# Performance work log

Hardware: AMD Instinct MI355X
Metric: run time of the kernel (lower is better)

## Reference

```python
import jax, jax.numpy as jnp
import numpy as np

B, L, H, TE = 256, 2048, 64, 64  # batch, seq len, hidden_size, num_time_enc_dims


def _lin_init(k, out_d, in_d):
    bound = 1.0 / np.sqrt(in_d)
    kw, kb = jax.random.split(k)
    w = jax.random.uniform(kw, (out_d, in_d), jnp.float32, -bound, bound)
    b = jax.random.uniform(kb, (out_d,), jnp.float32, -bound, bound)
    return w, b


def setup_inputs() -> dict:
    key = jax.random.key(0)
    ks = jax.random.split(key, 16)
    x_xy = jax.random.normal(ks[0], (B, L, 2), jnp.float32)
    mask = jax.random.bernoulli(ks[1], 0.8, (B, L, 1)).astype(jnp.float32)  # 0 => masked position
    x = jnp.concatenate([x_xy, mask], axis=-1)  # (B,L,3)
    t = jax.random.uniform(ks[2], (B, L, 1), jnp.float32)
    te_w1, te_b1 = _lin_init(ks[3], TE, 1)
    te_w2, te_b2 = _lin_init(ks[4], TE, TE)
    fproj_w, fproj_b = _lin_init(ks[5], H, 3 + TE)
    bproj_w, bproj_b = _lin_init(ks[6], H, 3 + TE)
    fwz, fbz = _lin_init(ks[7], H, H)
    fwh, fbh = _lin_init(ks[8], H, H)
    bwz, bbz = _lin_init(ks[9], H, H)
    bwh, bbh = _lin_init(ks[10], H, H)
    head_hidden = max((2 * H + TE) // 2, 128)  # = 128
    gh_w1, gh_b1 = _lin_init(ks[11], head_hidden, 2 * H + TE)
    gh_w2, gh_b2 = _lin_init(ks[12], 1, head_hidden)
    mask_token = jnp.array([0.0, 0.01], jnp.float32) + jnp.array([0.1, 0.001], jnp.float32) * jax.random.normal(ks[13], (2,), jnp.float32)
    return dict(x=x, t=t, mask_token=mask_token,
                te_w1=te_w1, te_b1=te_b1, te_w2=te_w2, te_b2=te_b2,
                fproj_w=fproj_w, fproj_b=fproj_b, bproj_w=bproj_w, bproj_b=bproj_b,
                fwz=fwz, fbz=fbz, fwh=fwh, fbh=fbh,
                bwz=bwz, bbz=bbz, bwh=bwh, bbh=bbh,
                gh_w1=gh_w1, gh_b1=gh_b1, gh_w2=gh_w2, gh_b2=gh_b2)


def _mingru_prestates(inp, wz, bz, wh, bh, reverse):
    # inp: (B,L,H). Returns the hidden state BEFORE each step's update, in
    # time order, matching the torch code which stores h_* before cell.step.
    z = jax.nn.sigmoid(jnp.einsum('blh,oh->blo', inp, wz) + bz)
    h_tilde = jnp.tanh(jnp.einsum('blh,oh->blo', inp, wh) + bh)

    def step(h, zh):
        z_t, ht_t = zh
        return (1.0 - z_t) * h + z_t * ht_t, h  # emit pre-update carry

    h0 = jnp.zeros((inp.shape[0], wz.shape[0]), inp.dtype)
    _, hs = jax.lax.scan(step, h0,
                         (jnp.swapaxes(z, 0, 1), jnp.swapaxes(h_tilde, 0, 1)),
                         reverse=reverse)
    return jnp.swapaxes(hs, 0, 1)  # (B,L,H)


def reference(x, t, mask_token,
              te_w1, te_b1, te_w2, te_b2,
              fproj_w, fproj_b, bproj_w, bproj_b,
              fwz, fbz, fwh, fbh,
              bwz, bbz, bwh, bbh,
              gh_w1, gh_b1, gh_w2, gh_b2):
    mask_chan = x[..., 2:3]                      # (B,L,1)
    masked_pos = mask_chan == 0
    x_first2 = jnp.where(masked_pos, mask_token.reshape(1, 1, 2), x[..., :2])
    x3 = jnp.concatenate([x_first2, mask_chan], axis=-1)  # (B,L,3)

    t_enc = jax.nn.relu(jnp.einsum('blk,ok->blo', t, te_w1) + te_b1)
    t_enc = jnp.einsum('blk,ok->blo', t_enc, te_w2) + te_b2  # (B,L,TE)

    x_cat = jnp.concatenate([x3, t_enc], axis=-1)  # (B,L,3+TE)

    inp_fwd = jnp.einsum('blk,ok->blo', x_cat, fproj_w) + fproj_b
    inp_bwd = jnp.einsum('blk,ok->blo', x_cat, bproj_w) + bproj_b

    h_fwd = _mingru_prestates(inp_fwd, fwz, fbz, fwh, fbh, reverse=False)  # state after steps 0..t-1
    h_bwd = _mingru_prestates(inp_bwd, bwz, bbz, bwh, bbh, reverse=True)   # state after steps L-1..t+1

    h_fwd_final = h_fwd[:, -1:, :]  # state after steps 0..L-2
    h_bwd_final = h_bwd[:, 0:1, :]  # state after steps L-1..1

    unmasked = mask_chan > 0
    h_fwd_apply = jnp.where(unmasked, h_fwd, h_fwd_final)
    h_bwd_apply = jnp.where(unmasked, h_bwd, h_bwd_final)

    h_bi = jnp.concatenate([h_fwd_apply, h_bwd_apply, t_enc], axis=-1)  # (B,L,2H+TE)
    hid = jax.nn.relu(jnp.einsum('blk,ok->blo', h_bi, gh_w1) + gh_b1)
    preds = jnp.einsum('blk,ok->blo', hid, gh_w2) + gh_b2  # (B,L,1)
    return preds
```

## Files before the change

### kernel.cpp

```cpp
#include <hip/hip_runtime.h>
#include <stdint.h>

#define NB 256
#define NL 2048

typedef __attribute__((ext_vector_type(8))) short short8;
typedef __attribute__((ext_vector_type(4))) float f32x4;
#define MFMA16(a,b,c) __builtin_amdgcn_mfma_f32_16x16x32_bf16(a,b,c,0,0,0)

static __device__ __forceinline__ unsigned short f2bf(float f) {
    union { float f; uint32_t u; } v; v.f = f;
    uint32_t u = v.u;
    uint32_t r = u + 0x7fffu + ((u >> 16) & 1u);
    return (unsigned short)(r >> 16);
}
static __device__ __forceinline__ float bflo(uint32_t u) {
    union { uint32_t u; float f; } v; v.u = u << 16; return v.f;
}
static __device__ __forceinline__ float bfhi(uint32_t u) {
    union { uint32_t u; float f; } v; v.u = u & 0xffff0000u; return v.f;
}
#if __has_builtin(__builtin_amdgcn_cvt_pk_bf16_f32)
typedef __attribute__((ext_vector_type(2))) __bf16 bf16x2_t;
static __device__ __forceinline__ uint32_t pk2(float lo, float hi) {
    union { bf16x2_t v; uint32_t u; } c;
    c.v = __builtin_amdgcn_cvt_pk_bf16_f32(lo, hi);
    return c.u;
}
static __device__ __forceinline__ unsigned short bf1(float v) {
    union { bf16x2_t v; uint32_t u; } c;
    c.v = __builtin_amdgcn_cvt_pk_bf16_f32(v, v);
    return (unsigned short)(c.u & 0xffffu);
}
#else
static __device__ __forceinline__ uint32_t pk2(float lo, float hi) {
    return ((uint32_t)f2bf(hi) << 16) | (uint32_t)f2bf(lo);
}
static __device__ __forceinline__ unsigned short bf1(float v) { return f2bf(v); }
#endif
static __device__ __forceinline__ short8 frag8(const float* p) {
    short8 r;
#pragma unroll
    for (int j = 0; j < 8; ++j) r[j] = (short)f2bf(p[j]);
    return r;
}

static __device__ __forceinline__ void barrier_lds() {
    asm volatile("s_waitcnt lgkmcnt(0)" ::: "memory");
    __builtin_amdgcn_s_barrier();
}

__global__ __launch_bounds__(256, 3) void prep_kernel(
    const float* __restrict__ x, const float* __restrict__ t,
    const float* __restrict__ mtok,
    const float* __restrict__ te_w1, const float* __restrict__ te_b1,
    const float* __restrict__ te_w2, const float* __restrict__ te_b2,
    const float* __restrict__ fpw, const float* __restrict__ fpb,
    const float* __restrict__ bpw, const float* __restrict__ bpb,
    int b0,
    unsigned short* __restrict__ inpF,
    unsigned short* __restrict__ inpB)
{
    __shared__ __align__(16) unsigned short s_te1[64*72];
    __shared__ __align__(16) unsigned short s_tenc[64*72];
    __shared__ __align__(16) unsigned short s_xa[64*40];
    __shared__ __align__(16) unsigned short s_inp[2][64*72];

    const int tid = threadIdx.x;
    const int w   = tid >> 6;
    const int l   = tid & 63;
    const int lq  = l >> 4;
    const int ln  = l & 15;

    short8 bte[2];
    {
        const float* row = te_w2 + (w*16 + ln)*64;
#pragma unroll
        for (int ks = 0; ks < 2; ++ks) bte[ks] = frag8(row + lq*8 + ks*32);
    }
    short8 bpj[2][3];
#pragma unroll
    for (int p = 0; p < 2; ++p) {
        const int g = 2*w + p;
        const float* PW = (g < 4) ? fpw : bpw;
        const float* row = PW + ((g & 3)*16 + ln)*67;
#pragma unroll
        for (int ks = 0; ks < 2; ++ks) {
            float tmp[8];
#pragma unroll
            for (int j = 0; j < 8; ++j) tmp[j] = row[3 + lq*8 + ks*32 + j];
            bpj[p][ks] = frag8(tmp);
        }
        {
            float tmp[8];
#pragma unroll
            for (int j = 0; j < 8; ++j) tmp[j] = (lq == 0 && j < 3) ? row[j] : 0.f;
            bpj[p][2] = frag8(tmp);
        }
    }
    const float bias_te = te_b2[w*16 + ln];
    float bias_pj[2];
#pragma unroll
    for (int p = 0; p < 2; ++p) {
        const int g = 2*w + p;
        bias_pj[p] = ((g < 4) ? fpb : bpb)[(g & 3)*16 + ln];
    }
    const float mt0 = mtok[0], mt1 = mtok[1];

    const int baseposl = blockIdx.x * 256;

    auto P0 = [&](int ch) {
        const int gbase = (b0 << 11) + baseposl + ch*64;
        const int pos = tid & 63;
        const float tv = t[gbase + pos];
        const int k0 = (tid >> 6) * 16;
        uint32_t* dst = (uint32_t*)(s_te1 + pos*72 + k0);
#pragma unroll
        for (int kk = 0; kk < 16; kk += 2) {
            float v0 = fmaxf(fmaf(tv, te_w1[k0+kk],   te_b1[k0+kk]),   0.f);
            float v1 = fmaxf(fmaf(tv, te_w1[k0+kk+1], te_b1[k0+kk+1]), 0.f);
            dst[kk >> 1] = pk2(v0, v1);
        }
        if (tid < 64) {
            const float* xp = x + (size_t)(gbase + tid)*3;
            const float mc = xp[2];
            const float x0 = (mc == 0.f) ? mt0 : xp[0];
            const float x1 = (mc == 0.f) ? mt1 : xp[1];
            uint32_t* xr = (uint32_t*)(s_xa + tid*40);
            xr[0] = pk2(x0, x1);
            xr[1] = pk2(mc, 0.f);
        }
    };
    auto G1 = [&]() {
        const int o = w*16 + ln;
#pragma unroll
        for (int mt = 0; mt < 4; ++mt) {
            f32x4 c = {0.f, 0.f, 0.f, 0.f};
#pragma unroll
            for (int ks = 0; ks < 2; ++ks) {
                const short8 a = *(const short8*)(s_te1 + (mt*16+ln)*72 + lq*8 + ks*32);
                c = MFMA16(a, bte[ks], c);
            }
#pragma unroll
            for (int r = 0; r < 4; ++r) {
                const int m = mt*16 + lq*4 + r;
                s_tenc[m*72 + o] = bf1(c[r] + bias_te);
            }
        }
    };
    auto G2 = [&]() {
#pragma unroll
        for (int mt = 0; mt < 4; ++mt) {
            short8 a0 = *(const short8*)(s_tenc + (mt*16+ln)*72 + lq*8);
            short8 a1 = *(const short8*)(s_tenc + (mt*16+ln)*72 + lq*8 + 32);
            short8 a2 = *(const short8*)(s_xa   + (mt*16+ln)*40 + lq*8);
#pragma unroll
            for (int p = 0; p < 2; ++p) {
                const int g = 2*w + p;
                const int dir = g >> 2;
                const int o = (g & 3)*16 + ln;
                f32x4 c = {0.f, 0.f, 0.f, 0.f};
                c = MFMA16(a0, bpj[p][0], c);
                c = MFMA16(a1, bpj[p][1], c);
                c = MFMA16(a2, bpj[p][2], c);
#pragma unroll
                for (int r = 0; r < 4; ++r) {
                    const int m = mt*16 + lq*4 + r;
                    s_inp[dir][m*72 + o] = bf1(c[r] + bias_pj[p]);
                }
            }
        }
    };
    auto S = [&](int ch) {
        const int chbase = baseposl + ch*64;
        const int ll0 = chbase & 2047;
        const int bl  = chbase >> 11;
        uint32_t* dstF = (uint32_t*)inpF + ((size_t)bl*NL + ll0)*32;
        uint32_t* dstB = (uint32_t*)inpB + ((size_t)bl*NL + ll0)*32;
        const uint32_t* srcW = (const uint32_t*)s_inp;
#pragma unroll
        for (int rep = 0; rep < 16; ++rep) {
            const int idx = rep*256 + tid;
            const int d   = idx >> 11;
            const int rem = idx & 2047;
            const int ll  = rem >> 5;
            const int dw  = rem & 31;
            const uint32_t v = srcW[d*2304 + ll*36 + dw];
            (d ? dstB : dstF)[ll*32 + dw] = v;
        }
    };

#pragma unroll
    for (int i = tid; i < 64*20; i += 256) {
        if ((i % 20) >= 2) ((uint32_t*)s_xa)[i] = 0;
    }
    P0(0);
    barrier_lds();
    G1();
    barrier_lds();
    G2();
    barrier_lds();
#pragma unroll 1
    for (int ch = 0; ch < 4; ++ch) {
        S(ch);
        if (ch < 3) P0(ch + 1);
        barrier_lds();
        if (ch < 3) {
            G1();
            barrier_lds();
            G2();
            barrier_lds();
        }
    }
}

#define SSTR 129

__global__ __launch_bounds__(512, 2) void scan3_kernel(
    const unsigned short* __restrict__ inpf, const unsigned short* __restrict__ inpb,
    const float* __restrict__ fwz, const float* __restrict__ fbz,
    const float* __restrict__ fwh, const float* __restrict__ fbh,
    const float* __restrict__ bwz, const float* __restrict__ bbz,
    const float* __restrict__ bwh, const float* __restrict__ bbh,
    unsigned short* __restrict__ hf, unsigned short* __restrict__ hb)
{
    __shared__ uint32_t s_seg[64*SSTR];
    __shared__ float s_A[8][65], s_B[8][65], s_Hin[8][65];
    __shared__ float s_H[64];

    const int rl  = blockIdx.x >> 1;
    const int dir = blockIdx.x & 1;
    const int tid = threadIdx.x;
    const int h   = tid & 63;
    const int q   = tid >> 6;
    const int lq  = h >> 4;
    const int ln  = h & 15;

    const unsigned short* inp = (dir ? inpb : inpf) + (size_t)rl * NL * 64;
    unsigned short* out = (dir ? hb : hf) + (size_t)rl * NL * 64;

    const float* WZ = dir ? bwz : fwz;
    const float* WH = dir ? bwh : fwh;
    const float* BZ = dir ? bbz : fbz;
    const float* BH = dir ? bbh : fbh;

    short8 bz[4][2], bh[4][2];
    float biz[4], bih[4];
#pragma unroll
    for (int nt = 0; nt < 4; ++nt) {
        const float* rz = WZ + (nt*16 + ln)*64;
        const float* rh = WH + (nt*16 + ln)*64;
#pragma unroll
        for (int ks = 0; ks < 2; ++ks) {
            bz[nt][ks] = frag8(rz + lq*8 + ks*32);
            bh[nt][ks] = frag8(rh + lq*8 + ks*32);
        }
        biz[nt] = BZ[nt*16 + ln];
        bih[nt] = BH[nt*16 + ln];
    }

    if (tid < 64) s_H[tid] = 0.f;

    short8 a0c, a1c;
    {
        const int s0 = dir ? 15 : 0;
        const unsigned short* p = inp + (size_t)(s0*128 + q*16 + ln)*64 + lq*8;
        a0c = *(const short8*)(p);
        a1c = *(const short8*)(p + 32);
    }
    short8 a0n = a0c, a1n = a1c;
    barrier_lds();

#pragma unroll 1
    for (int si = 0; si < 16; ++si) {
        const int s = dir ? (15 - si) : si;
        if (si < 15) {
            const int sn = dir ? (14 - si) : (si + 1);
            const unsigned short* p = inp + (size_t)(sn*128 + q*16 + ln)*64 + lq*8;
            a0n = *(const short8*)(p);
            a1n = *(const short8*)(p + 32);
        }
#pragma unroll
        for (int nt = 0; nt < 4; ++nt) {
            f32x4 cz  = {0.f, 0.f, 0.f, 0.f};
            f32x4 ch2 = {0.f, 0.f, 0.f, 0.f};
            cz  = MFMA16(a0c, bz[nt][0], cz);
            cz  = MFMA16(a1c, bz[nt][1], cz);
            ch2 = MFMA16(a0c, bh[nt][0], ch2);
            ch2 = MFMA16(a1c, bh[nt][1], ch2);
#pragma unroll
            for (int r = 0; r < 4; ++r) {
                const float az = cz[r]  + biz[nt];
                const float ah = ch2[r] + bih[nt];
                const float z  = __builtin_amdgcn_rcpf(1.f + __expf(-az));
                const float cc = fminf(fmaxf(ah, -15.f), 15.f);
                const float e2 = __expf(2.f * cc);
                const float th = 1.f - 2.f * __builtin_amdgcn_rcpf(e2 + 1.f);
                s_seg[(nt*16 + ln)*SSTR + q*16 + lq*4 + r] = pk2(1.f - z, z * th);
            }
        }
        barrier_lds();

        uint32_t regs[16];
        float A = 1.f, Bc = 0.f;
#pragma unroll
        for (int i = 0; i < 16; ++i) {
            const int g = q*16 + i;
            const int xx = dir ? (127 - g) : g;
            const uint32_t uab = s_seg[h*SSTR + xx];
            regs[i] = uab;
            Bc = fmaf(bflo(uab), Bc, bfhi(uab));
            A *= bflo(uab);
        }
        s_A[q][h] = A; s_B[q][h] = Bc;
        barrier_lds();

        if (tid < 64) {
            float H = s_H[tid];
#pragma unroll
            for (int qq = 0; qq < 8; ++qq) {
                s_Hin[qq][tid] = H;
                H = fmaf(s_A[qq][tid], H, s_B[qq][tid]);
            }
            s_H[tid] = H;
        }
        barrier_lds();

        float hv = s_Hin[q][h];
        const int l0 = s * 128;
#pragma unroll
        for (int i = 0; i < 16; ++i) {
            const int g = q*16 + i;
            const int xx = dir ? (127 - g) : g;
            const uint32_t uab = regs[i];
            out[(size_t)(l0 + xx)*64 + h] = bf1(hv);
            hv = fmaf(bflo(uab), hv, bfhi(uab));
        }
        barrier_lds();
        a0c = a0n; a1c = a1n;
    }
}

__global__ __launch_bounds__(256, 3) void head_kernel(
    const float* __restrict__ x, const float* __restrict__ t,
    const float* __restrict__ te_w1, const float* __restrict__ te_b1,
    const float* __restrict__ te_w2, const float* __restrict__ te_b2,
    const unsigned short* __restrict__ hf, const unsigned short* __restrict__ hb,
    const float* __restrict__ w1, const float* __restrict__ b1,
    const float* __restrict__ w2, const float* __restrict__ b2,
    int b0,
    float* __restrict__ out)
{
    __shared__ __align__(16) unsigned short s_a[64*200];
    __shared__ __align__(16) unsigned short s_te1[64*72];
    __shared__ float s_part[4][64];
    __shared__ float s_mc[64];

    const int tid = threadIdx.x;
    const int w   = tid >> 6;
    const int l   = tid & 63;
    const int lq  = l >> 4;
    const int ln  = l & 15;

    short8 bw1[2][6];
    float b1v[2], w2v[2];
#pragma unroll
    for (int p = 0; p < 2; ++p) {
        const int o = (2*w + p)*16 + ln;
        const float* row = w1 + o*192;
#pragma unroll
        for (int ks = 0; ks < 6; ++ks) bw1[p][ks] = frag8(row + lq*8 + ks*32);
        b1v[p] = b1[o];
        w2v[p] = w2[o];
    }
    short8 bte[2];
    {
        const float* row = te_w2 + (w*16 + ln)*64;
#pragma unroll
        for (int ks = 0; ks < 2; ++ks) bte[ks] = frag8(row + lq*8 + ks*32);
    }
    const float bias_te = te_b2[w*16 + ln];
    const float bias2 = b2[0];

    const int baseposl = blockIdx.x * 256;

    auto A = [&](int ch) {
        const int gbase = (b0 << 11) + baseposl + ch*64;
        if (tid < 64) s_mc[tid] = x[(size_t)(gbase + tid)*3 + 2];
        const int pos = tid & 63;
        const float tv = t[gbase + pos];
        const int k0 = (tid >> 6) * 16;
        uint32_t* dst = (uint32_t*)(s_te1 + pos*72 + k0);
#pragma unroll
        for (int kk = 0; kk < 16; kk += 2) {
            float v0 = fmaxf(fmaf(tv, te_w1[k0+kk],   te_b1[k0+kk]),   0.f);
            float v1 = fmaxf(fmaf(tv, te_w1[k0+kk+1], te_b1[k0+kk+1]), 0.f);
            dst[kk >> 1] = pk2(v0, v1);
        }
    };
    auto Bp = [&](int ch) {
        const int chbase = baseposl + ch*64;
        const int ll0 = chbase & 2047;
        const int bl  = chbase >> 11;
        const size_t rowbase = (size_t)bl * NL * 64;
#pragma unroll
        for (int rep = 0; rep < 4; ++rep) {
            const int idx = rep*256 + tid;
            const int seg = idx >> 9;
            const int row = (idx >> 3) & 63;
            const int c   = idx & 7;
            const bool unm = s_mc[row] > 0.f;
            const uint4* src = (seg == 0)
                ? (const uint4*)(hf + rowbase + (size_t)(unm ? (ll0+row) : (NL-1))*64)
                : (const uint4*)(hb + rowbase + (size_t)(unm ? (ll0+row) : 0)*64);
            ((uint4*)s_a)[row*25 + seg*8 + c] = src[c];
        }
        const int o = w*16 + ln;
#pragma unroll
        for (int mt = 0; mt < 4; ++mt) {
            f32x4 c = {0.f, 0.f, 0.f, 0.f};
#pragma unroll
            for (int ks = 0; ks < 2; ++ks) {
                const short8 a = *(const short8*)(s_te1 + (mt*16+ln)*72 + lq*8 + ks*32);
                c = MFMA16(a, bte[ks], c);
            }
#pragma unroll
            for (int r = 0; r < 4; ++r) {
                const int m = mt*16 + lq*4 + r;
                s_a[m*200 + 128 + o] = bf1(c[r] + bias_te);
            }
        }
    };
    auto Cp = [&]() {
#pragma unroll
        for (int mt = 0; mt < 4; ++mt) {
            short8 af[6];
#pragma unroll
            for (int ks = 0; ks < 6; ++ks)
                af[ks] = *(const short8*)(s_a + (mt*16+ln)*200 + lq*8 + ks*32);
            float vs[4] = {0.f, 0.f, 0.f, 0.f};
#pragma unroll
            for (int p = 0; p < 2; ++p) {
                f32x4 c = {0.f, 0.f, 0.f, 0.f};
#pragma unroll
                for (int ks = 0; ks < 6; ++ks) c = MFMA16(af[ks], bw1[p][ks], c);
#pragma unroll
                for (int r = 0; r < 4; ++r)
                    vs[r] += fmaxf(c[r] + b1v[p], 0.f) * w2v[p];
            }
#pragma unroll
            for (int mask = 1; mask < 16; mask <<= 1) {
#pragma unroll
                for (int r = 0; r < 4; ++r)
                    vs[r] += __shfl_xor(vs[r], mask);
            }
            if (ln == 0) {
#pragma unroll
                for (int r = 0; r < 4; ++r)
                    s_part[w][mt*16 + lq*4 + r] = vs[r];
            }
        }
    };
    auto Dp = [&](int ch) {
        const int gbase = (b0 << 11) + baseposl + ch*64;
        if (tid < 64) {
            out[gbase + tid] = s_part[0][tid] + s_part[1][tid]
                             + s_part[2][tid] + s_part[3][tid] + bias2;
        }
    };

    A(0);
    barrier_lds();
#pragma unroll 1
    for (int ch = 0; ch < 4; ++ch) {
        Bp(ch);
        barrier_lds();
        Cp();
        barrier_lds();
        Dp(ch);
        if (ch < 3) A(ch + 1);
        barrier_lds();
    }
}

extern "C" void kernel_launch(void* const* d_in, const int* in_sizes, int n_in,
                              void* d_out, int out_size, void* d_ws, size_t ws_size,
                              hipStream_t stream)
{
    const float* x     = (const float*)d_in[0];
    const float* t     = (const float*)d_in[1];
    const float* mtok  = (const float*)d_in[2];
    const float* te_w1 = (const float*)d_in[3];
    const float* te_b1 = (const float*)d_in[4];
    const float* te_w2 = (const float*)d_in[5];
    const float* te_b2 = (const float*)d_in[6];
    const float* fpw   = (const float*)d_in[7];
    const float* fpb   = (const float*)d_in[8];
    const float* bpw   = (const float*)d_in[9];
    const float* bpb   = (const float*)d_in[10];
    const float* fwz   = (const float*)d_in[11];
    const float* fbz   = (const float*)d_in[12];
    const float* fwh   = (const float*)d_in[13];
    const float* fbh   = (const float*)d_in[14];
    const float* bwz   = (const float*)d_in[15];
    const float* bbz   = (const float*)d_in[16];
    const float* bwh   = (const float*)d_in[17];
    const float* bbh   = (const float*)d_in[18];
    const float* w1    = (const float*)d_in[19];
    const float* b1    = (const float*)d_in[20];
    const float* w2    = (const float*)d_in[21];
    const float* b2    = (const float*)d_in[22];

    const size_t per_b = 1048576ull;
    int Bg = NB;
    while ((size_t)Bg * per_b > ws_size && Bg > 1) Bg >>= 1;
    const int nG = NB / Bg;

    char* ws = (char*)d_ws;
    unsigned short* inpf = (unsigned short*)ws;
    unsigned short* inpb = inpf + (size_t)Bg * NL * 64;
    unsigned short* hf   = inpb + (size_t)Bg * NL * 64;
    unsigned short* hb   = hf   + (size_t)Bg * NL * 64;

    for (int g = 0; g < nG; ++g) {
        const int b0 = g * Bg;

        prep_kernel<<<8 * Bg, 256, 0, stream>>>(
            x, t, mtok, te_w1, te_b1, te_w2, te_b2,
            fpw, fpb, bpw, bpb, b0, inpf, inpb);

        scan3_kernel<<<2 * Bg, 512, 0, stream>>>(
            inpf, inpb, fwz, fbz, fwh, fbh, bwz, bbz, bwh, bbh, hf, hb);

        head_kernel<<<8 * Bg, 256, 0, stream>>>(
            x, t, te_w1, te_b1, te_w2, te_b2,
            hf, hb, w1, b1, w2, b2, b0, (float*)d_out);
    }
}
```

Measured before the change: 334.4 us.

## Fuse time-encoding and input projection into the scan kernel

Removes the separate prep kernel: each scan block now computes the time encoding and the forward or backward input projection for its own 128-position segment with MFMA, then feeds the gate computation directly from LDS. This drops the bf16 intermediate inpF/inpB round-trip through global memory and halves workspace. The loop is also restructured into a software pipeline: the previous segment's state writeback and the next segment's projection overlap with the current scan, and one barrier per step is removed. In exchange the scan blocks do the time-encoding work redundantly for both directions and hold more registers, which may lower occupancy.

```diff
diff --git a/kernel.cpp b/kernel.cpp
--- a/kernel.cpp
+++ b/kernel.cpp
@@ -50,182 +50,26 @@
     __builtin_amdgcn_s_barrier();
 }
 
-__global__ __launch_bounds__(256, 3) void prep_kernel(
+#define SSTR 129
+
+__global__ __launch_bounds__(512, 2) void scan_fused(
     const float* __restrict__ x, const float* __restrict__ t,
     const float* __restrict__ mtok,
     const float* __restrict__ te_w1, const float* __restrict__ te_b1,
     const float* __restrict__ te_w2, const float* __restrict__ te_b2,
     const float* __restrict__ fpw, const float* __restrict__ fpb,
     const float* __restrict__ bpw, const float* __restrict__ bpb,
-    int b0,
-    unsigned short* __restrict__ inpF,
-    unsigned short* __restrict__ inpB)
-{
-    __shared__ __align__(16) unsigned short s_te1[64*72];
-    __shared__ __align__(16) unsigned short s_tenc[64*72];
-    __shared__ __align__(16) unsigned short s_xa[64*40];
-    __shared__ __align__(16) unsigned short s_inp[2][64*72];
-
-    const int tid = threadIdx.x;
-    const int w   = tid >> 6;
-    const int l   = tid & 63;
-    const int lq  = l >> 4;
-    const int ln  = l & 15;
-
-    short8 bte[2];
-    {
-        const float* row = te_w2 + (w*16 + ln)*64;
-#pragma unroll
-        for (int ks = 0; ks < 2; ++ks) bte[ks] = frag8(row + lq*8 + ks*32);
-    }
-    short8 bpj[2][3];
-#pragma unroll
-    for (int p = 0; p < 2; ++p) {
-        const int g = 2*w + p;
-        const float* PW = (g < 4) ? fpw : bpw;
-        const float* row = PW + ((g & 3)*16 + ln)*67;
-#pragma unroll
-        for (int ks = 0; ks < 2; ++ks) {
-            float tmp[8];
-#pragma unroll
-            for (int j = 0; j < 8; ++j) tmp[j] = row[3 + lq*8 + ks*32 + j];
-            bpj[p][ks] = frag8(tmp);
-        }
-        {
-            float tmp[8];
-#pragma unroll
-            for (int j = 0; j < 8; ++j) tmp[j] = (lq == 0 && j < 3) ? row[j] : 0.f;
-            bpj[p][2] = frag8(tmp);
-        }
-    }
-    const float bias_te = te_b2[w*16 + ln];
-    float bias_pj[2];
-#pragma unroll
-    for (int p = 0; p < 2; ++p) {
-        const int g = 2*w + p;
-        bias_pj[p] = ((g < 4) ? fpb : bpb)[(g & 3)*16 + ln];
-    }
-    const float mt0 = mtok[0], mt1 = mtok[1];
-
-    const int baseposl = blockIdx.x * 256;
-
-    auto P0 = [&](int ch) {
-        const int gbase = (b0 << 11) + baseposl + ch*64;
-        const int pos = tid & 63;
-        const float tv = t[gbase + pos];
-        const int k0 = (tid >> 6) * 16;
-        uint32_t* dst = (uint32_t*)(s_te1 + pos*72 + k0);
-#pragma unroll
-        for (int kk = 0; kk < 16; kk += 2) {
-            float v0 = fmaxf(fmaf(tv, te_w1[k0+kk],   te_b1[k0+kk]),   0.f);
-            float v1 = fmaxf(fmaf(tv, te_w1[k0+kk+1], te_b1[k0+kk+1]), 0.f);
-            dst[kk >> 1] = pk2(v0, v1);
-        }
-        if (tid < 64) {
-            const float* xp = x + (size_t)(gbase + tid)*3;
-            const float mc = xp[2];
-            const float x0 = (mc == 0.f) ? mt0 : xp[0];
-            const float x1 = (mc == 0.f) ? mt1 : xp[1];
-            uint32_t* xr = (uint32_t*)(s_xa + tid*40);
-            xr[0] = pk2(x0, x1);
-            xr[1] = pk2(mc, 0.f);
-        }
-    };
-    auto G1 = [&]() {
-        const int o = w*16 + ln;
-#pragma unroll
-        for (int mt = 0; mt < 4; ++mt) {
-            f32x4 c = {0.f, 0.f, 0.f, 0.f};
-#pragma unroll
-            for (int ks = 0; ks < 2; ++ks) {
-                const short8 a = *(const short8*)(s_te1 + (mt*16+ln)*72 + lq*8 + ks*32);
-                c = MFMA16(a, bte[ks], c);
-            }
-#pragma unroll
-            for (int r = 0; r < 4; ++r) {
-                const int m = mt*16 + lq*4 + r;
-                s_tenc[m*72 + o] = bf1(c[r] + bias_te);
-            }
-        }
-    };
-    auto G2 = [&]() {
-#pragma unroll
-        for (int mt = 0; mt < 4; ++mt) {
-            short8 a0 = *(const short8*)(s_tenc + (mt*16+ln)*72 + lq*8);
-            short8 a1 = *(const short8*)(s_tenc + (mt*16+ln)*72 + lq*8 + 32);
-            short8 a2 = *(const short8*)(s_xa   + (mt*16+ln)*40 + lq*8);
-#pragma unroll
-            for (int p = 0; p < 2; ++p) {
-                const int g = 2*w + p;
-                const int dir = g >> 2;
-                const int o = (g & 3)*16 + ln;
-                f32x4 c = {0.f, 0.f, 0.f, 0.f};
-                c = MFMA16(a0, bpj[p][0], c);
-                c = MFMA16(a1, bpj[p][1], c);
-                c = MFMA16(a2, bpj[p][2], c);
-#pragma unroll
-                for (int r = 0; r < 4; ++r) {
-                    const int m = mt*16 + lq*4 + r;
-                    s_inp[dir][m*72 + o] = bf1(c[r] + bias_pj[p]);
-                }
-            }
-        }
-    };
-    auto S = [&](int ch) {
-        const int chbase = baseposl + ch*64;
-        const int ll0 = chbase & 2047;
-        const int bl  = chbase >> 11;
-        uint32_t* dstF = (uint32_t*)inpF + ((size_t)bl*NL + ll0)*32;
-        uint32_t* dstB = (uint32_t*)inpB + ((size_t)bl*NL + ll0)*32;
-        const uint32_t* srcW = (const uint32_t*)s_inp;
-#pragma unroll
-        for (int rep = 0; rep < 16; ++rep) {
-            const int idx = rep*256 + tid;
-            const int d   = idx >> 11;
-            const int rem = idx & 2047;
-            const int ll  = rem >> 5;
-            const int dw  = rem & 31;
-            const uint32_t v = srcW[d*2304 + ll*36 + dw];
-            (d ? dstB : dstF)[ll*32 + dw] = v;
-        }
-    };
-
-#pragma unroll
-    for (int i = tid; i < 64*20; i += 256) {
-        if ((i % 20) >= 2) ((uint32_t*)s_xa)[i] = 0;
-    }
-    P0(0);
-    barrier_lds();
-    G1();
-    barrier_lds();
-    G2();
-    barrier_lds();
-#pragma unroll 1
-    for (int ch = 0; ch < 4; ++ch) {
-        S(ch);
-        if (ch < 3) P0(ch + 1);
-        barrier_lds();
-        if (ch < 3) {
-            G1();
-            barrier_lds();
-            G2();
-            barrier_lds();
-        }
-    }
-}
-
-#define SSTR 129
-
-__global__ __launch_bounds__(512, 2) void scan3_kernel(
-    const unsigned short* __restrict__ inpf, const unsigned short* __restrict__ inpb,
     const float* __restrict__ fwz, const float* __restrict__ fbz,
     const float* __restrict__ fwh, const float* __restrict__ fbh,
     const float* __restrict__ bwz, const float* __restrict__ bbz,
     const float* __restrict__ bwh, const float* __restrict__ bbh,
+    int b0,
     unsigned short* __restrict__ hf, unsigned short* __restrict__ hb)
 {
+    __shared__ __align__(16) unsigned short s_tenc[128*72];
+    __shared__ __align__(16) unsigned short s_inp[128*72];
     __shared__ uint32_t s_seg[64*SSTR];
-    __shared__ float s_A[8][65], s_B[8][65], s_Hin[8][65];
+    __shared__ float s_A[8][65], s_B[8][65];
     __shared__ float s_H[64];
 
     const int rl  = blockIdx.x >> 1;
@@ -236,14 +80,53 @@
     const int lq  = h >> 4;
     const int ln  = h & 15;
 
-    const unsigned short* inp = (dir ? inpb : inpf) + (size_t)rl * NL * 64;
+    const int gx = (b0 + rl) << 11;
     unsigned short* out = (dir ? hb : hf) + (size_t)rl * NL * 64;
 
+    float w1v[16], b1v[16];
+#pragma unroll
+    for (int ks = 0; ks < 2; ++ks)
+#pragma unroll
+        for (int j = 0; j < 8; ++j) {
+            const int k = lq*8 + ks*32 + j;
+            w1v[ks*8+j] = te_w1[k];
+            b1v[ks*8+j] = te_b1[k];
+        }
+    short8 bte[4][2];
+    float bite[4];
+#pragma unroll
+    for (int nt = 0; nt < 4; ++nt) {
+        const float* row = te_w2 + (nt*16 + ln)*64;
+#pragma unroll
+        for (int ks = 0; ks < 2; ++ks) bte[nt][ks] = frag8(row + lq*8 + ks*32);
+        bite[nt] = te_b2[nt*16 + ln];
+    }
+    const float* PW = dir ? bpw : fpw;
+    const float* PB = dir ? bpb : fpb;
+    short8 bpj[4][3];
+    float bipj[4];
+#pragma unroll
+    for (int nt = 0; nt < 4; ++nt) {
+        const float* row = PW + (nt*16 + ln)*67;
+#pragma unroll
+        for (int ks = 0; ks < 2; ++ks) {
+            float tmp[8];
+#pragma unroll
+            for (int j = 0; j < 8; ++j) tmp[j] = row[3 + lq*8 + ks*32 + j];
+            bpj[nt][ks] = frag8(tmp);
+        }
+        {
+            float tmp[8];
+#pragma unroll
+            for (int j = 0; j < 8; ++j) tmp[j] = (lq == 0 && j < 3) ? row[j] : 0.f;
+            bpj[nt][2] = frag8(tmp);
+        }
+        bipj[nt] = PB[nt*16 + ln];
+    }
     const float* WZ = dir ? bwz : fwz;
     const float* WH = dir ? bwh : fwh;
     const float* BZ = dir ? bbz : fbz;
     const float* BH = dir ? bbh : fbh;
-
     short8 bz[4][2], bh[4][2];
     float biz[4], bih[4];
 #pragma unroll
@@ -258,36 +141,60 @@
         biz[nt] = BZ[nt*16 + ln];
         bih[nt] = BH[nt*16 + ln];
     }
-
-    if (tid < 64) s_H[tid] = 0.f;
-
-    short8 a0c, a1c;
-    {
-        const int s0 = dir ? 15 : 0;
-        const unsigned short* p = inp + (size_t)(s0*128 + q*16 + ln)*64 + lq*8;
-        a0c = *(const short8*)(p);
-        a1c = *(const short8*)(p + 32);
-    }
-    short8 a0n = a0c, a1n = a1c;
-    barrier_lds();
-
-#pragma unroll 1
-    for (int si = 0; si < 16; ++si) {
-        const int s = dir ? (15 - si) : si;
-        if (si < 15) {
-            const int sn = dir ? (14 - si) : (si + 1);
-            const unsigned short* p = inp + (size_t)(sn*128 + q*16 + ln)*64 + lq*8;
-            a0n = *(const short8*)(p);
-            a1n = *(const short8*)(p + 32);
-        }
+    const float mt0 = mtok[0], mt1 = mtok[1];
+
+    auto G1 = [&](float tv) {
+        short8 a[2];
+#pragma unroll
+        for (int ks = 0; ks < 2; ++ks)
+#pragma unroll
+            for (int j = 0; j < 8; ++j) {
+                const float v = fmaxf(fmaf(tv, w1v[ks*8+j], b1v[ks*8+j]), 0.f);
+                a[ks][j] = (short)bf1(v);
+            }
+#pragma unroll
+        for (int nt = 0; nt < 4; ++nt) {
+            f32x4 c = {0.f, 0.f, 0.f, 0.f};
+            c = MFMA16(a[0], bte[nt][0], c);
+            c = MFMA16(a[1], bte[nt][1], c);
+#pragma unroll
+            for (int r = 0; r < 4; ++r)
+                s_tenc[(q*16 + lq*4 + r)*72 + nt*16 + ln] = bf1(c[r] + bite[nt]);
+        }
+    };
+    auto G2 = [&](float xx0, float xx1, float mc) {
+        const short8 a0 = *(const short8*)(s_tenc + (q*16+ln)*72 + lq*8);
+        const short8 a1 = *(const short8*)(s_tenc + (q*16+ln)*72 + lq*8 + 32);
+        short8 a2 = {0,0,0,0,0,0,0,0};
+        if (lq == 0) {
+            const float x0m = (mc == 0.f) ? mt0 : xx0;
+            const float x1m = (mc == 0.f) ? mt1 : xx1;
+            a2[0] = (short)bf1(x0m);
+            a2[1] = (short)bf1(x1m);
+            a2[2] = (short)bf1(mc);
+        }
+#pragma unroll
+        for (int nt = 0; nt < 4; ++nt) {
+            f32x4 c = {0.f, 0.f, 0.f, 0.f};
+            c = MFMA16(a0, bpj[nt][0], c);
+            c = MFMA16(a1, bpj[nt][1], c);
+            c = MFMA16(a2, bpj[nt][2], c);
+#pragma unroll
+            for (int r = 0; r < 4; ++r)
+                s_inp[(q*16 + lq*4 + r)*72 + nt*16 + ln] = bf1(c[r] + bipj[nt]);
+        }
+    };
+    auto GATES = [&]() {
+        const short8 a0 = *(const short8*)(s_inp + (q*16+ln)*72 + lq*8);
+        const short8 a1 = *(const short8*)(s_inp + (q*16+ln)*72 + lq*8 + 32);
 #pragma unroll
         for (int nt = 0; nt < 4; ++nt) {
             f32x4 cz  = {0.f, 0.f, 0.f, 0.f};
             f32x4 ch2 = {0.f, 0.f, 0.f, 0.f};
-            cz  = MFMA16(a0c, bz[nt][0], cz);
-            cz  = MFMA16(a1c, bz[nt][1], cz);
-            ch2 = MFMA16(a0c, bh[nt][0], ch2);
-            ch2 = MFMA16(a1c, bh[nt][1], ch2);
+            cz  = MFMA16(a0, bz[nt][0], cz);
+            cz  = MFMA16(a1, bz[nt][1], cz);
+            ch2 = MFMA16(a0, bh[nt][0], ch2);
+            ch2 = MFMA16(a1, bh[nt][1], ch2);
 #pragma unroll
             for (int r = 0; r < 4; ++r) {
                 const float az = cz[r]  + biz[nt];
@@ -299,45 +206,93 @@
                 s_seg[(nt*16 + ln)*SSTR + q*16 + lq*4 + r] = pk2(1.f - z, z * th);
             }
         }
-        barrier_lds();
-
-        uint32_t regs[16];
-        float A = 1.f, Bc = 0.f;
+    };
+
+    if (tid < 64) s_H[tid] = 0.f;
+
+    const int s0 = dir ? 15 : 0;
+    G1(t[gx + s0*128 + q*16 + ln]);
+    barrier_lds();
+    float xr0 = 0.f, xr1 = 0.f, xmc = 0.f;
+    if (lq == 0) {
+        const float* xp = x + (size_t)(gx + s0*128 + q*16 + ln)*3;
+        xr0 = xp[0]; xr1 = xp[1]; xmc = xp[2];
+    }
+    G2(xr0, xr1, xmc);
+    const int s1 = dir ? 14 : 1;
+    float tvn = t[gx + s1*128 + q*16 + ln];
+    if (lq == 0) {
+        const float* xp = x + (size_t)(gx + s1*128 + q*16 + ln)*3;
+        xr0 = xp[0]; xr1 = xp[1]; xmc = xp[2];
+    }
+    barrier_lds();
+
+    uint32_t regs[16];
+    int l0p = 0;
+
+#pragma unroll 1
+    for (int si = 0; si < 16; ++si) {
+        const int s = dir ? (15 - si) : si;
+        if (si > 0) {
+            float hv = s_A[q][h];
+#pragma unroll
+            for (int i = 0; i < 16; ++i) {
+                const int g = q*16 + i;
+                const int xx = dir ? (127 - g) : g;
+                out[(size_t)(l0p + xx)*64 + h] = bf1(hv);
+                hv = fmaf(bflo(regs[i]), hv, bfhi(regs[i]));
+            }
+        }
+        GATES();
+        barrier_lds();
+        {
+            float A = 1.f, Bc = 0.f;
+#pragma unroll
+            for (int i = 0; i < 16; ++i) {
+                const int g = q*16 + i;
+                const int xx = dir ? (127 - g) : g;
+                const uint32_t uab = s_seg[h*SSTR + xx];
+                regs[i] = uab;
+                Bc = fmaf(bflo(uab), Bc, bfhi(uab));
+                A *= bflo(uab);
+            }
+            s_A[q][h] = A; s_B[q][h] = Bc;
+        }
+        if (si < 15) G1(tvn);
+        barrier_lds();
+        if (tid < 64) {
+            float H = s_H[tid];
+#pragma unroll
+            for (int qq = 0; qq < 8; ++qq) {
+                const float a = s_A[qq][tid], b = s_B[qq][tid];
+                s_A[qq][tid] = H;
+                H = fmaf(a, H, b);
+            }
+            s_H[tid] = H;
+        }
+        if (si < 15) {
+            G2(xr0, xr1, xmc);
+            if (si < 14) {
+                const int s2 = dir ? (13 - si) : (si + 2);
+                tvn = t[gx + s2*128 + q*16 + ln];
+                if (lq == 0) {
+                    const float* xp = x + (size_t)(gx + s2*128 + q*16 + ln)*3;
+                    xr0 = xp[0]; xr1 = xp[1]; xmc = xp[2];
+                }
+            }
+        }
+        barrier_lds();
+        l0p = s * 128;
+    }
+    {
+        float hv = s_A[q][h];
 #pragma unroll
         for (int i = 0; i < 16; ++i) {
             const int g = q*16 + i;
             const int xx = dir ? (127 - g) : g;
-            const uint32_t uab = s_seg[h*SSTR + xx];
-            regs[i] = uab;
-            Bc = fmaf(bflo(uab), Bc, bfhi(uab));
-            A *= bflo(uab);
-        }
-        s_A[q][h] = A; s_B[q][h] = Bc;
-        barrier_lds();
-
-        if (tid < 64) {
-            float H = s_H[tid];
-#pragma unroll
-            for (int qq = 0; qq < 8; ++qq) {
-                s_Hin[qq][tid] = H;
-                H = fmaf(s_A[qq][tid], H, s_B[qq][tid]);
-            }
-            s_H[tid] = H;
-        }
-        barrier_lds();
-
-        float hv = s_Hin[q][h];
-        const int l0 = s * 128;
-#pragma unroll
-        for (int i = 0; i < 16; ++i) {
-            const int g = q*16 + i;
-            const int xx = dir ? (127 - g) : g;
-            const uint32_t uab = regs[i];
-            out[(size_t)(l0 + xx)*64 + h] = bf1(hv);
-            hv = fmaf(bflo(uab), hv, bfhi(uab));
-        }
-        barrier_lds();
-        a0c = a0n; a1c = a1n;
+            out[(size_t)(l0p + xx)*64 + h] = bf1(hv);
+            hv = fmaf(bflo(regs[i]), hv, bfhi(regs[i]));
+        }
     }
 }
 
@@ -511,26 +466,22 @@
     const float* w2    = (const float*)d_in[21];
     const float* b2    = (const float*)d_in[22];
 
-    const size_t per_b = 1048576ull;
+    const size_t per_b = 524288ull;
     int Bg = NB;
     while ((size_t)Bg * per_b > ws_size && Bg > 1) Bg >>= 1;
     const int nG = NB / Bg;
 
     char* ws = (char*)d_ws;
-    unsigned short* inpf = (unsigned short*)ws;
-    unsigned short* inpb = inpf + (size_t)Bg * NL * 64;
-    unsigned short* hf   = inpb + (size_t)Bg * NL * 64;
-    unsigned short* hb   = hf   + (size_t)Bg * NL * 64;
+    unsigned short* hf = (unsigned short*)ws;
+    unsigned short* hb = hf + (size_t)Bg * NL * 64;
 
     for (int g = 0; g < nG; ++g) {
         const int b0 = g * Bg;
 
-        prep_kernel<<<8 * Bg, 256, 0, stream>>>(
+        scan_fused<<<2 * Bg, 512, 0, stream>>>(
             x, t, mtok, te_w1, te_b1, te_w2, te_b2,
-            fpw, fpb, bpw, bpb, b0, inpf, inpb);
-
-        scan3_kernel<<<2 * Bg, 512, 0, stream>>>(
-            inpf, inpb, fwz, fbz, fwh, fbh, bwz, bbz, bwh, bbh, hf, hb);
+            fpw, fpb, bpw, bpb, fwz, fbz, fwh, fbh, bwz, bbz, bwh, bbh,
+            b0, hf, hb);
 
         head_kernel<<<8 * Bg, 256, 0, stream>>>(
             x, t, te_w1, te_b1, te_w2, te_b2,
```

After: 484.5 us. 1.45x slower.
